# Performance work log

Hardware: AMD Instinct MI355X
Metric: run time of the kernel (lower is better)

## Reference

```python
import jax, jax.numpy as jnp
import numpy as np

B, S, DK = 32, 2048, 64

def setup_inputs() -> dict:
    key = jax.random.key(0)
    kq, kk, kv = jax.random.split(key, 3)
    Q = jax.random.normal(kq, (B, S, DK), dtype=jnp.float32)
    K = jax.random.normal(kk, (B, S, DK), dtype=jnp.float32)
    V = jax.random.normal(kv, (B, S, DK), dtype=jnp.float32)
    return {"Q": Q, "K": K, "V": V}

def reference(Q, K, V):
    # attn_scores = Q K^T / sqrt(d_k); full [B,S,S] probs materialized (naive, non-flash)
    d_k = Q.shape[-1]
    scores = jnp.einsum('bqd,bkd->bqk', Q, K) / jnp.sqrt(jnp.asarray(d_k, Q.dtype))
    probs = jax.nn.softmax(scores, axis=-1)
    return jnp.einsum('bqk,bkd->bqd', probs, V)
```

## Files before the change

### kernel.cpp

```cpp
#include <hip/hip_runtime.h>
#include <hip/hip_bf16.h>

#define BATCH 32
#define SEQ   2048
#define DKK   64

constexpr int QT  = 128;
constexpr int KT  = 64;
constexpr int NW  = 4;
constexpr int NIT = SEQ / KT;
constexpr int LST = 66;

typedef __attribute__((ext_vector_type(8)))  short bf16x8;
typedef __attribute__((ext_vector_type(16))) float f32x16;

__device__ __forceinline__ unsigned cvt2(float a, float b) {
    union { __hip_bfloat162 h; unsigned u; } c;
    c.h = __float22bfloat162_rn(make_float2(a, b));
    return c.u;
}

__device__ __forceinline__ float fast_exp2(float x) {
#if __has_builtin(__builtin_amdgcn_exp2f)
    return __builtin_amdgcn_exp2f(x);
#else
    return exp2f(x);
#endif
}

__global__ __launch_bounds__(256, 2) void attn_fwd(
        const float* __restrict__ Q, const float* __restrict__ K,
        const float* __restrict__ V, float* __restrict__ O) {
    __shared__ short Kb[2][KT][LST];
    __shared__ short Vt[2][DKK][LST];
    __shared__ short Pb[NW][32][LST];

    const int tid  = threadIdx.x;
    const int w    = tid >> 6;
    const int lane = tid & 63;
    const int hi   = lane >> 5;
    const int l31  = lane & 31;
    const int b    = blockIdx.y;
    const int q0   = blockIdx.x * QT + w * 32;

    const float qscale = 0.125f * 1.44269504088896340736f;
    bf16x8 qfrag[4];
    #pragma unroll
    for (int c = 0; c < 4; ++c) {
        const float* qp = Q + ((size_t)b * SEQ + q0 + l31) * DKK + 16*c + 8*hi;
        float4 a  = *(const float4*)qp;
        float4 a2 = *(const float4*)(qp + 4);
        union { bf16x8 v; unsigned u[4]; } f;
        f.u[0] = cvt2(a.x*qscale,  a.y*qscale);
        f.u[1] = cvt2(a.z*qscale,  a.w*qscale);
        f.u[2] = cvt2(a2.x*qscale, a2.y*qscale);
        f.u[3] = cvt2(a2.z*qscale, a2.w*qscale);
        qfrag[c] = f.v;
    }

    f32x16 o0 = {}, o1 = {};
    float lsum = 0.f;

    const float* Kbase = K + (size_t)b * SEQ * DKK;
    const float* Vbase = V + (size_t)b * SEQ * DKK;

    const int krow0 = tid >> 4;
    const int kcol  = (tid & 15) << 2;
    const int vd    = tid & 63;
    const int vg    = (tid >> 6) << 4;

    float4 kp[4];
    float  vp[16];
    auto load_regs = [&](int t) {
        const float* Kg = Kbase + (size_t)(t * KT) * DKK;
        #pragma unroll
        for (int i = 0; i < 4; ++i)
            kp[i] = *(const float4*)(Kg + (size_t)(krow0 + 16*i) * DKK + kcol);
        const float* Vg = Vbase + (size_t)(t * KT + vg) * DKK + vd;
        #pragma unroll
        for (int i = 0; i < 16; ++i) vp[i] = Vg[(size_t)i * DKK];
    };
    auto write_lds = [&](int buf) {
        #pragma unroll
        for (int i = 0; i < 4; ++i) {
            int2 kk;
            kk.x = (int)cvt2(kp[i].x, kp[i].y);
            kk.y = (int)cvt2(kp[i].z, kp[i].w);
            *(int2*)&Kb[buf][krow0 + 16*i][kcol] = kk;
        }
        union { bf16x8 v; unsigned u[4]; } t0, t1;
        t0.u[0] = cvt2(vp[0],  vp[1]);  t0.u[1] = cvt2(vp[2],  vp[3]);
        t0.u[2] = cvt2(vp[4],  vp[5]);  t0.u[3] = cvt2(vp[6],  vp[7]);
        t1.u[0] = cvt2(vp[8],  vp[9]);  t1.u[1] = cvt2(vp[10], vp[11]);
        t1.u[2] = cvt2(vp[12], vp[13]); t1.u[3] = cvt2(vp[14], vp[15]);
        *(bf16x8*)&Vt[buf][vd][vg]     = t0.v;
        *(bf16x8*)&Vt[buf][vd][vg + 8] = t1.v;
    };

    load_regs(0);
    write_lds(0);
    load_regs(1);
    __syncthreads();

    for (int it = 0; it < NIT; ++it) {
        const int cur = it & 1;

        #pragma unroll
        for (int kt2 = 0; kt2 < 2; ++kt2) {
            f32x16 acc = {};
            #pragma unroll
            for (int c = 0; c < 4; ++c) {
                bf16x8 kf = *(const bf16x8*)&Kb[cur][32*kt2 + l31][16*c + 8*hi];
                acc = __builtin_amdgcn_mfma_f32_32x32x16_bf16(kf, qfrag[c], acc, 0, 0, 0);
            }
            float p[16];
            #pragma unroll
            for (int r = 0; r < 16; ++r) { p[r] = fast_exp2(acc[r]); lsum += p[r]; }
            #pragma unroll
            for (int G = 0; G < 4; ++G) {
                int2 pw;
                pw.x = (int)cvt2(p[4*G],     p[4*G + 1]);
                pw.y = (int)cvt2(p[4*G + 2], p[4*G + 3]);
                *(int2*)&Pb[w][l31][32*kt2 + 8*G + 4*hi] = pw;
            }
        }

        #pragma unroll
        for (int c = 0; c < 4; ++c) {
            bf16x8 pf  = *(const bf16x8*)&Pb[w][l31][16*c + 8*hi];
            bf16x8 vf0 = *(const bf16x8*)&Vt[cur][l31     ][16*c + 8*hi];
            bf16x8 vf1 = *(const bf16x8*)&Vt[cur][32 + l31][16*c + 8*hi];
            o0 = __builtin_amdgcn_mfma_f32_32x32x16_bf16(vf0, pf, o0, 0, 0, 0);
            o1 = __builtin_amdgcn_mfma_f32_32x32x16_bf16(vf1, pf, o1, 0, 0, 0);
        }

        if (it + 1 < NIT) {
            write_lds(1 - cur);
            if (it + 2 < NIT) load_regs(it + 2);
            __syncthreads();
        }
    }

    float s = lsum;
    s += __shfl_xor(s, 32);
    const float inv = 1.0f / s;

    float* op = O + ((size_t)b * SEQ + q0 + l31) * DKK;
    #pragma unroll
    for (int G = 0; G < 4; ++G) {
        float4 st;
        st.x = o0[4*G + 0] * inv; st.y = o0[4*G + 1] * inv;
        st.z = o0[4*G + 2] * inv; st.w = o0[4*G + 3] * inv;
        *(float4*)(op + 8*G + 4*hi) = st;
        st.x = o1[4*G + 0] * inv; st.y = o1[4*G + 1] * inv;
        st.z = o1[4*G + 2] * inv; st.w = o1[4*G + 3] * inv;
        *(float4*)(op + 32 + 8*G + 4*hi) = st;
    }
}

extern "C" void kernel_launch(void* const* d_in, const int* in_sizes, int n_in,
                              void* d_out, int out_size, void* d_ws, size_t ws_size,
                              hipStream_t stream) {
    const float* Q = (const float*)d_in[0];
    const float* K = (const float*)d_in[1];
    const float* V = (const float*)d_in[2];
    float* O = (float*)d_out;
    dim3 grid(SEQ / QT, BATCH);
    attn_fwd<<<grid, dim3(256), 0, stream>>>(Q, K, V, O);
}
```

Baseline: 140.0 us.

## Keep P in registers via permlane32 swap and remap blocks across XCDs

Replaces the per-wave LDS round trip for the probability tile with an in-register transpose built from permlane32_swap. The converted P fragments then feed the PV MFMAs directly, and the PV matmul is interleaved into each half-tile. This drops the P LDS writes and reads and frees the Pb shared buffer. Block indices are also remapped so consecutive blocks on each XCD share a batch, which should improve L2 reuse of K and V. The risk is that the lane permutation must exactly reproduce the previous MFMA operand layout.

```diff
diff --git a/kernel.cpp b/kernel.cpp
--- a/kernel.cpp
+++ b/kernel.cpp
@@ -7,12 +7,12 @@
 
 constexpr int QT  = 128;
 constexpr int KT  = 64;
-constexpr int NW  = 4;
 constexpr int NIT = SEQ / KT;
 constexpr int LST = 66;
 
 typedef __attribute__((ext_vector_type(8)))  short bf16x8;
 typedef __attribute__((ext_vector_type(16))) float f32x16;
+typedef __attribute__((ext_vector_type(2)))  unsigned uint2v;
 
 __device__ __forceinline__ unsigned cvt2(float a, float b) {
     union { __hip_bfloat162 h; unsigned u; } c;
@@ -33,15 +33,17 @@
         const float* __restrict__ V, float* __restrict__ O) {
     __shared__ short Kb[2][KT][LST];
     __shared__ short Vt[2][DKK][LST];
-    __shared__ short Pb[NW][32][LST];
 
     const int tid  = threadIdx.x;
     const int w    = tid >> 6;
     const int lane = tid & 63;
     const int hi   = lane >> 5;
     const int l31  = lane & 31;
-    const int b    = blockIdx.y;
-    const int q0   = blockIdx.x * QT + w * 32;
+
+    const int lin  = (int)blockIdx.x + ((int)blockIdx.y << 4);
+    const int work = ((lin & 7) << 6) | (lin >> 3);
+    const int b    = work >> 4;
+    const int q0   = (work & 15) * QT + w * 32;
 
     const float qscale = 0.125f * 1.44269504088896340736f;
     bf16x8 qfrag[4];
@@ -116,22 +118,28 @@
             float p[16];
             #pragma unroll
             for (int r = 0; r < 16; ++r) { p[r] = fast_exp2(acc[r]); lsum += p[r]; }
+
+            unsigned pw0 = cvt2(p[0],  p[1]),  pw1 = cvt2(p[2],  p[3]);
+            unsigned pw2 = cvt2(p[4],  p[5]),  pw3 = cvt2(p[6],  p[7]);
+            unsigned pw4 = cvt2(p[8],  p[9]),  pw5 = cvt2(p[10], p[11]);
+            unsigned pw6 = cvt2(p[12], p[13]), pw7 = cvt2(p[14], p[15]);
+            uint2v s02 = __builtin_amdgcn_permlane32_swap(pw0, pw2, false, false);
+            uint2v s13 = __builtin_amdgcn_permlane32_swap(pw1, pw3, false, false);
+            uint2v s46 = __builtin_amdgcn_permlane32_swap(pw4, pw6, false, false);
+            uint2v s57 = __builtin_amdgcn_permlane32_swap(pw5, pw7, false, false);
+            union { bf16x8 v; unsigned u[4]; } pa0, pa1;
+            pa0.u[0] = s02[0]; pa0.u[1] = s13[0]; pa0.u[2] = s02[1]; pa0.u[3] = s13[1];
+            pa1.u[0] = s46[0]; pa1.u[1] = s57[0]; pa1.u[2] = s46[1]; pa1.u[3] = s57[1];
+
             #pragma unroll
-            for (int G = 0; G < 4; ++G) {
-                int2 pw;
-                pw.x = (int)cvt2(p[4*G],     p[4*G + 1]);
-                pw.y = (int)cvt2(p[4*G + 2], p[4*G + 3]);
-                *(int2*)&Pb[w][l31][32*kt2 + 8*G + 4*hi] = pw;
+            for (int cc = 0; cc < 2; ++cc) {
+                const int c = 2*kt2 + cc;
+                bf16x8 pf  = cc ? pa1.v : pa0.v;
+                bf16x8 vf0 = *(const bf16x8*)&Vt[cur][l31     ][16*c + 8*hi];
+                bf16x8 vf1 = *(const bf16x8*)&Vt[cur][32 + l31][16*c + 8*hi];
+                o0 = __builtin_amdgcn_mfma_f32_32x32x16_bf16(vf0, pf, o0, 0, 0, 0);
+                o1 = __builtin_amdgcn_mfma_f32_32x32x16_bf16(vf1, pf, o1, 0, 0, 0);
             }
-        }
-
-        #pragma unroll
-        for (int c = 0; c < 4; ++c) {
-            bf16x8 pf  = *(const bf16x8*)&Pb[w][l31][16*c + 8*hi];
-            bf16x8 vf0 = *(const bf16x8*)&Vt[cur][l31     ][16*c + 8*hi];
-            bf16x8 vf1 = *(const bf16x8*)&Vt[cur][32 + l31][16*c + 8*hi];
-            o0 = __builtin_amdgcn_mfma_f32_32x32x16_bf16(vf0, pf, o0, 0, 0, 0);
-            o1 = __builtin_amdgcn_mfma_f32_32x32x16_bf16(vf1, pf, o1, 0, 0, 0);
         }
 
         if (it + 1 < NIT) {
```

Result: faster. 135.8 us (-3.0%).
